# Optimization experiments

Hardware: AMD Instinct MI355X
Metric: run time of the kernel (lower is better)

The kernel has to match this reference:

```python
import jax, jax.numpy as jnp
import numpy as np

N_HEAD = 16

def setup_inputs() -> dict:
    key = jax.random.key(0)
    k1, k2, k3 = jax.random.split(key, 3)
    B, K, C = 2, 2048, 1024
    x = jax.random.normal(k1, (B, K, C), dtype=jnp.float32)
    W_qkv = jax.random.normal(k2, (C, 3 * C), dtype=jnp.float32) * (1.0 / np.sqrt(C))
    b_qkv = jnp.zeros((3 * C,), dtype=jnp.float32)
    W_proj = jax.random.normal(k3, (C, C), dtype=jnp.float32) * (1.0 / np.sqrt(C))
    b_proj = jnp.zeros((C,), dtype=jnp.float32)
    return {"x": x, "W_qkv": W_qkv, "b_qkv": b_qkv, "W_proj": W_proj, "b_proj": b_proj, "K": K}

def reference(x, W_qkv, b_qkv, W_proj, b_proj, K):
    B, _, C = x.shape
    H = N_HEAD
    Dh = C // H
    qkv = x @ W_qkv + b_qkv                      # [B, K, 3C]
    q, k, v = jnp.split(qkv, 3, axis=-1)
    # [B, H, K, Dh]
    q = q.reshape(B, K, H, Dh).transpose(0, 2, 1, 3)
    k = k.reshape(B, K, H, Dh).transpose(0, 2, 1, 3)
    v = v.reshape(B, K, H, Dh).transpose(0, 2, 1, 3)
    att = jnp.einsum('bhqd,bhkd->bhqk', q, k) / jnp.sqrt(jnp.asarray(Dh, dtype=x.dtype))
    causal = jnp.tril(jnp.ones((K, K), dtype=bool))
    att = jnp.where(causal[None, None], att, jnp.asarray(-jnp.inf, dtype=x.dtype))
    att = jax.nn.softmax(att, axis=-1)
    y = jnp.einsum('bhqk,bhkd->bhqd', att, v)    # [B, H, K, Dh]
    y = y.transpose(0, 2, 1, 3).reshape(B, K, C)
    return y @ W_proj + b_proj
```

## Files before the change

kernel.cpp:

```cpp
#include <hip/hip_runtime.h>
#include <hip/hip_bf16.h>
#include <math.h>

typedef __attribute__((ext_vector_type(8))) short short8;
typedef __attribute__((ext_vector_type(4))) float f32x4;
typedef __attribute__((ext_vector_type(4))) short short4v;
typedef __attribute__((ext_vector_type(2))) int int2v;

static __device__ __forceinline__ short f2bf(float f) {
    __hip_bfloat16 h = __float2bfloat16(f);
    return *reinterpret_cast<short*>(&h);
}
static __device__ __forceinline__ void store_out(float* p, float v) { *p = v; }
static __device__ __forceinline__ void store_out(short* p, float v) { *p = f2bf(v); }

#define GLL16(g, l) __builtin_amdgcn_global_load_lds( \
    (const __attribute__((address_space(1))) void*)(g), \
    (__attribute__((address_space(3))) void*)(l), 16, 0, 0)

#if __has_builtin(__builtin_amdgcn_exp2f)
#define EXP2(x) __builtin_amdgcn_exp2f(x)
#else
#define EXP2(x) exp2f(x)
#endif

#if __has_builtin(__builtin_amdgcn_cvt_pk_bf16_f32)
typedef __attribute__((ext_vector_type(2))) __bf16 bf16x2;
static __device__ __forceinline__ int pack2bf(float a, float b) {
    bf16x2 r = __builtin_amdgcn_cvt_pk_bf16_f32(a, b);
    return __builtin_bit_cast(int, r);
}
#else
static __device__ __forceinline__ int pack2bf(float a, float b) {
    unsigned ua = __builtin_bit_cast(unsigned, a) + 0x8000u;
    unsigned ub = __builtin_bit_cast(unsigned, b) + 0x8000u;
    return (int)((ua >> 16) | (ub & 0xFFFF0000u));
}
#endif

struct BTrue  { static constexpr bool v = true;  };
struct BFalse { static constexpr bool v = false; };

__global__ __launch_bounds__(256) void cast_bf16_kernel(
    const float* __restrict__ in, short* __restrict__ out, int n)
{
    int i = (blockIdx.x * 256 + threadIdx.x) * 4;
    if (i >= n) return;
    float4 v = *(const float4*)(in + i);
    short4v o = { f2bf(v.x), f2bf(v.y), f2bf(v.z), f2bf(v.w) };
    *(short4v*)(out + i) = o;
}

__global__ __launch_bounds__(256) void transpose_cast_kernel(
    const float* __restrict__ W, short* __restrict__ Wt, int Kd, int N)
{
    __shared__ float ts[32][33];
    const int c0 = blockIdx.x * 32, r0 = blockIdx.y * 32;
    const int tx = threadIdx.x & 31, ty = threadIdx.x >> 5;
    #pragma unroll
    for (int e = 0; e < 4; ++e)
        ts[ty + e * 8][tx] = W[(size_t)(r0 + ty + e * 8) * N + c0 + tx];
    __syncthreads();
    #pragma unroll
    for (int e = 0; e < 4; ++e)
        Wt[(size_t)(c0 + ty + e * 8) * Kd + r0 + tx] = f2bf(ts[tx][ty + e * 8]);
}

__global__ __launch_bounds__(256) void vtrans_kernel(
    const short* __restrict__ qkvb, short* __restrict__ vt, int K, int C)
{
    __shared__ short Vs[64][72];
    const int k0 = blockIdx.x * 64, h = blockIdx.y, b = blockIdx.z;
    const size_t rs = (size_t)3 * C;
    const short* src = qkvb + (size_t)b * K * rs + 2 * C + h * 64;
    const int key = threadIdx.x >> 3, d0 = (threadIdx.x & 7) * 8;
    *(short8*)&Vs[key][d0]      = *(const short8*)(src + (size_t)(k0 + key) * rs + d0);
    *(short8*)&Vs[key + 32][d0] = *(const short8*)(src + (size_t)(k0 + key + 32) * rs + d0);
    __syncthreads();
    const int d = threadIdx.x >> 2, kc = threadIdx.x & 3;
    short* dst = vt + ((size_t)(b * 16 + h) * 64 + d) * K + k0 + kc * 16;
    short8 o0, o1;
    #pragma unroll
    for (int j = 0; j < 8; ++j) { o0[j] = Vs[kc * 16 + j][d]; o1[j] = Vs[kc * 16 + 8 + j][d]; }
    *(short8*)dst = o0;
    *(short8*)(dst + 8) = o1;
}

#define GM 128
#define GN 128
#define GK 32

template <typename OutT>
__global__ __launch_bounds__(256) void gemm_mfma_kernel(
    const short* __restrict__ A, const short* __restrict__ Bt,
    const float* __restrict__ bias, OutT* __restrict__ C,
    int M, int N, int Kd)
{
    __shared__ __attribute__((aligned(16))) short As[GM * GK];
    __shared__ __attribute__((aligned(16))) short Bs[GN * GK];
    const int tid  = threadIdx.x;
    const int lane = tid & 63, w = tid >> 6;
    const int col  = lane & 15, quad = lane >> 4;
    const int wm = (w & 1) * 64, wn = (w >> 1) * 64;
    const int row0 = blockIdx.y * GM, col0 = blockIdx.x * GN;

    const int sr = tid >> 2, sc = (tid & 3) * 8;
    const short* gA = A  + (size_t)(row0 + sr) * Kd + sc;
    const short* gB = Bt + (size_t)(col0 + sr) * Kd + sc;
    short* lA = As + sr * GK + sc;
    short* lB = Bs + sr * GK + sc;
    const size_t skip = (size_t)64 * Kd;

    f32x4 acc[4][4] = {};
    for (int k0 = 0; k0 < Kd; k0 += GK) {
        __syncthreads();
        GLL16(gA,        lA);
        GLL16(gA + skip, lA + 64 * GK);
        GLL16(gB,        lB);
        GLL16(gB + skip, lB + 64 * GK);
        gA += GK; gB += GK;
        __syncthreads();

        short8 aF[4], bF[4];
        #pragma unroll
        for (int mt = 0; mt < 4; ++mt)
            aF[mt] = *(const short8*)&As[(wm + mt * 16 + col) * GK + quad * 8];
        #pragma unroll
        for (int nt = 0; nt < 4; ++nt)
            bF[nt] = *(const short8*)&Bs[(wn + nt * 16 + col) * GK + quad * 8];
        #pragma unroll
        for (int mt = 0; mt < 4; ++mt)
            #pragma unroll
            for (int nt = 0; nt < 4; ++nt)
                acc[mt][nt] = __builtin_amdgcn_mfma_f32_16x16x32_bf16(aF[mt], bF[nt], acc[mt][nt], 0, 0, 0);
    }

    #pragma unroll
    for (int mt = 0; mt < 4; ++mt)
        #pragma unroll
        for (int i = 0; i < 4; ++i) {
            const size_t r = row0 + wm + mt * 16 + quad * 4 + i;
            #pragma unroll
            for (int nt = 0; nt < 4; ++nt) {
                const int c = col0 + wn + nt * 16 + col;
                store_out(&C[r * N + c], acc[mt][nt][i] + bias[c]);
            }
        }
}

#define DH 64
#define FKT 64

__global__ __launch_bounds__(256) void flash_mfma_kernel(
    const short* __restrict__ qkvb,
    const short* __restrict__ vt,
    short* __restrict__ y,
    int K, int C)
{
    __shared__ __attribute__((aligned(16))) short Ks2[2 * 64 * 32];
    __shared__ __attribute__((aligned(16))) short Vs2[2 * 64 * 32];
    __shared__ __attribute__((aligned(16))) short Pt[4][16][72];

    const int tid  = threadIdx.x;
    const int lane = tid & 63, w = tid >> 6;
    const int col  = lane & 15, quad = lane >> 4;

    const int cmb  = blockIdx.x & 31;
    const int g    = blockIdx.x >> 5;
    const int b    = cmb >> 4, h = cmb & 15;
    const int NT   = K / 64;
    const float C2 = 0.18033688f;

    short8 bOnes;
    #pragma unroll
    for (int j = 0; j < 8; ++j) bOnes[j] = (col == 0) ? (short)0x3F80 : (short)0;

    const size_t rs = (size_t)3 * C;
    const short* qbase = qkvb + (size_t)b * K * rs + h * DH;
    const short* kbase = qbase + C;
    const short* vbase = vt + (size_t)(b * 16 + h) * DH * K;

    auto run = [&](int t0) {
        const int q0 = t0 + w * 16;

        short8 aQ0, aQ1;
        {
            const short* qp = qbase + (size_t)(q0 + col) * rs;
            aQ0 = *(const short8*)(qp + quad * 8);
            aQ1 = *(const short8*)(qp + 32 + quad * 8);
        }
        f32x4 O[4] = {};
        f32x4 L4 = {};

        const int nkt = t0 / FKT + 1;
        for (int it = 0; it < nkt; ++it) {
            const int kt = it * FKT;
            __syncthreads();
            #pragma unroll
            for (int cc = 0; cc < 2; ++cc) {
                const int seg  = w + 4 * cc;
                const int half = seg >> 2, kseg = seg & 3;
                const int rowl = kseg * 16 + (lane >> 2);
                const int grow = rowl ^ ((rowl >> 2) & 3);
                const int off  = half * 32 + (lane & 3) * 8;
                GLL16(kbase + (size_t)(kt + grow) * rs + off, &Ks2[seg * 512 + lane * 8]);
                GLL16(vbase + (size_t)rowl * K + kt + off,    &Vs2[seg * 512 + lane * 8]);
            }
            __syncthreads();

            f32x4 S[4] = {};
            #pragma unroll
            for (int nb = 0; nb < 4; ++nb) {
                const int prow = (col * 4 + nb) ^ (col & 3);
                short8 b0 = *(const short8*)&Ks2[prow * 32 + quad * 8];
                short8 b1 = *(const short8*)&Ks2[2048 + prow * 32 + quad * 8];
                S[nb] = __builtin_amdgcn_mfma_f32_16x16x32_bf16(aQ0, b0, S[nb], 0, 0, 0);
                S[nb] = __builtin_amdgcn_mfma_f32_16x16x32_bf16(aQ1, b1, S[nb], 0, 0, 0);
            }

            auto smax = [&](auto tag) {
                constexpr bool MASKED = decltype(tag)::v;
                #pragma unroll
                for (int i = 0; i < 4; ++i) {
                    const int q = q0 + quad * 4 + i;
                    float sv0 = S[0][i], sv1 = S[1][i], sv2 = S[2][i], sv3 = S[3][i];
                    if constexpr (MASKED) {
                        const int kc4 = kt + col * 4;
                        sv0 = (kc4 + 0 <= q) ? sv0 : -INFINITY;
                        sv1 = (kc4 + 1 <= q) ? sv1 : -INFINITY;
                        sv2 = (kc4 + 2 <= q) ? sv2 : -INFINITY;
                        sv3 = (kc4 + 3 <= q) ? sv3 : -INFINITY;
                    }
                    const float p0 = EXP2(sv0 * C2);
                    const float p1 = EXP2(sv1 * C2);
                    const float p2 = EXP2(sv2 * C2);
                    const float p3 = EXP2(sv3 * C2);
                    int2v pw = { pack2bf(p0, p1), pack2bf(p2, p3) };
                    *(int2v*)&Pt[w][quad * 4 + i][col * 4] = pw;
                }
            };
            if (kt + 63 <= q0) smax(BFalse{}); else smax(BTrue{});

            asm volatile("s_waitcnt lgkmcnt(0)" ::: "memory");

            #pragma unroll
            for (int half = 0; half < 2; ++half) {
                short8 aP = *(const short8*)&Pt[w][col][half * 32 + quad * 8];
                #pragma unroll
                for (int db = 0; db < 4; ++db) {
                    short8 bV = *(const short8*)&Vs2[half * 2048 + (db * 16 + col) * 32 + quad * 8];
                    O[db] = __builtin_amdgcn_mfma_f32_16x16x32_bf16(aP, bV, O[db], 0, 0, 0);
                }
                L4 = __builtin_amdgcn_mfma_f32_16x16x32_bf16(aP, bOnes, L4, 0, 0, 0);
            }
        }

        #pragma unroll
        for (int i = 0; i < 4; ++i) {
            const float l = __shfl(L4[i], quad * 16, 64);
            const float inv = 1.f / l;
            const int q = q0 + quad * 4 + i;
            short* yr = y + ((size_t)b * K + q) * C + h * DH;
            #pragma unroll
            for (int db = 0; db < 4; ++db)
                yr[db * 16 + col] = f2bf(O[db][i] * inv);
        }
    };

    run(g * 64);
    run((NT - 1 - g) * 64);
}

extern "C" void kernel_launch(void* const* d_in, const int* in_sizes, int n_in,
                              void* d_out, int out_size, void* d_ws, size_t ws_size,
                              hipStream_t stream)
{
    const float* x      = (const float*)d_in[0];
    const float* W_qkv  = (const float*)d_in[1];
    const float* b_qkv  = (const float*)d_in[2];
    const float* W_proj = (const float*)d_in[3];
    const float* b_proj = (const float*)d_in[4];

    const int B = 2, K = 2048, C = 1024, H = 16;
    const int M = B * K;

    char* ws = (char*)d_ws;
    short* xb    = (short*)ws;  ws += (size_t)M * C * 2;
    short* Wt1   = (short*)ws;  ws += (size_t)3 * C * C * 2;
    short* Wt2   = (short*)ws;  ws += (size_t)C * C * 2;
    short* qkvb  = (short*)ws;  ws += (size_t)M * 3 * C * 2;
    short* yb    = (short*)ws;  ws += (size_t)M * C * 2;
    short* vtb   = (short*)ws;

    cast_bf16_kernel<<<(M * C) / (256 * 4), 256, 0, stream>>>(x, xb, M * C);
    dim3 gt1((3 * C) / 32, C / 32);
    transpose_cast_kernel<<<gt1, 256, 0, stream>>>(W_qkv, Wt1, C, 3 * C);
    dim3 gt2(C / 32, C / 32);
    transpose_cast_kernel<<<gt2, 256, 0, stream>>>(W_proj, Wt2, C, C);

    dim3 g1((3 * C) / GN, M / GM);
    gemm_mfma_kernel<short><<<g1, 256, 0, stream>>>(xb, Wt1, b_qkv, qkvb, M, 3 * C, C);

    dim3 gv(K / 64, H, B);
    vtrans_kernel<<<gv, 256, 0, stream>>>(qkvb, vtb, K, C);

    const int NPAIR = (K / 64) / 2;
    flash_mfma_kernel<<<dim3(NPAIR * 32), 256, 0, stream>>>(qkvb, vtb, yb, K, C);

    dim3 g3(C / GN, M / GM);
    gemm_mfma_kernel<float><<<g3, 256, 0, stream>>>(yb, Wt2, b_proj, (float*)d_out, M, C, C);
}
```

Measured before the change: 194.5 us.

## Fuse prep kernels, fold softmax scale into QKV GEMM, widen flash warps to 32 queries

Merges the three input cast/transpose kernels into one launch to cut launch overhead. Folds the softmax scale (log2e/sqrt(Dh)) into the Q columns of the QKV GEMM epilogue, so the per-element multiply in the flash loop goes away. Restructures the flash kernel to 128 threads with each warp handling 32 query rows, so K/V fragments loaded from LDS are reused across two query groups. The cost is more registers per thread and fewer waves per block, which could hurt latency hiding; Q is also rounded to bf16 after scaling.

Result: slower. 207.3 us (+6.6%).

```diff
diff --git a/kernel.cpp b/kernel.cpp
--- a/kernel.cpp
+++ b/kernel.cpp
@@ -41,21 +41,12 @@
 struct BTrue  { static constexpr bool v = true;  };
 struct BFalse { static constexpr bool v = false; };
 
-__global__ __launch_bounds__(256) void cast_bf16_kernel(
-    const float* __restrict__ in, short* __restrict__ out, int n)
-{
-    int i = (blockIdx.x * 256 + threadIdx.x) * 4;
-    if (i >= n) return;
-    float4 v = *(const float4*)(in + i);
-    short4v o = { f2bf(v.x), f2bf(v.y), f2bf(v.z), f2bf(v.w) };
-    *(short4v*)(out + i) = o;
-}
-
-__global__ __launch_bounds__(256) void transpose_cast_kernel(
-    const float* __restrict__ W, short* __restrict__ Wt, int Kd, int N)
+static __device__ __forceinline__ void transpose_cast_tile(
+    const float* __restrict__ W, short* __restrict__ Wt, int Kd, int N,
+    int bx, int by)
 {
     __shared__ float ts[32][33];
-    const int c0 = blockIdx.x * 32, r0 = blockIdx.y * 32;
+    const int c0 = bx * 32, r0 = by * 32;
     const int tx = threadIdx.x & 31, ty = threadIdx.x >> 5;
     #pragma unroll
     for (int e = 0; e < 4; ++e)
@@ -64,6 +55,35 @@
     #pragma unroll
     for (int e = 0; e < 4; ++e)
         Wt[(size_t)(c0 + ty + e * 8) * Kd + r0 + tx] = f2bf(ts[tx][ty + e * 8]);
+}
+
+__global__ __launch_bounds__(256) void prep_kernel(
+    const float* __restrict__ x,      short* __restrict__ xb,    int nx,
+    const float* __restrict__ W_qkv,  short* __restrict__ Wt1,
+    const float* __restrict__ W_proj, short* __restrict__ Wt2,
+    int C)
+{
+    const int nbx = nx / 1024;
+    const int nb1 = (3 * C / 32) * (C / 32);
+    int bid = blockIdx.x;
+    if (bid < nbx) {
+        int i = (bid * 256 + threadIdx.x) * 4;
+        float4 v = *(const float4*)(x + i);
+        short4v o = { f2bf(v.x), f2bf(v.y), f2bf(v.z), f2bf(v.w) };
+        *(short4v*)(xb + i) = o;
+        return;
+    }
+    bid -= nbx;
+    if (bid < nb1) {
+        const int nc = 3 * C / 32;
+        transpose_cast_tile(W_qkv, Wt1, C, 3 * C, bid % nc, bid / nc);
+        return;
+    }
+    bid -= nb1;
+    {
+        const int nc = C / 32;
+        transpose_cast_tile(W_proj, Wt2, C, C, bid % nc, bid / nc);
+    }
 }
 
 __global__ __launch_bounds__(256) void vtrans_kernel(
@@ -94,7 +114,7 @@
 __global__ __launch_bounds__(256) void gemm_mfma_kernel(
     const short* __restrict__ A, const short* __restrict__ Bt,
     const float* __restrict__ bias, OutT* __restrict__ C,
-    int M, int N, int Kd)
+    int M, int N, int Kd, int qcols, float qscale)
 {
     __shared__ __attribute__((aligned(16))) short As[GM * GK];
     __shared__ __attribute__((aligned(16))) short Bs[GN * GK];
@@ -103,12 +123,13 @@
     const int col  = lane & 15, quad = lane >> 4;
     const int wm = (w & 1) * 64, wn = (w >> 1) * 64;
     const int row0 = blockIdx.y * GM, col0 = blockIdx.x * GN;
-
-    const int sr = tid >> 2, sc = (tid & 3) * 8;
-    const short* gA = A  + (size_t)(row0 + sr) * Kd + sc;
-    const short* gB = Bt + (size_t)(col0 + sr) * Kd + sc;
-    short* lA = As + sr * GK + sc;
-    short* lB = Bs + sr * GK + sc;
+    const float sc = (col0 < qcols) ? qscale : 1.f;
+
+    const int sr = tid >> 2, scg = (tid & 3) * 8;
+    const short* gA = A  + (size_t)(row0 + sr) * Kd + scg;
+    const short* gB = Bt + (size_t)(col0 + sr) * Kd + scg;
+    short* lA = As + sr * GK + scg;
+    short* lB = Bs + sr * GK + scg;
     const size_t skip = (size_t)64 * Kd;
 
     f32x4 acc[4][4] = {};
@@ -143,7 +164,7 @@
             #pragma unroll
             for (int nt = 0; nt < 4; ++nt) {
                 const int c = col0 + wn + nt * 16 + col;
-                store_out(&C[r * N + c], acc[mt][nt][i] + bias[c]);
+                store_out(&C[r * N + c], (acc[mt][nt][i] + bias[c]) * sc);
             }
         }
 }
@@ -151,7 +172,7 @@
 #define DH 64
 #define FKT 64
 
-__global__ __launch_bounds__(256) void flash_mfma_kernel(
+__global__ __launch_bounds__(128) void flash_mfma_kernel(
     const short* __restrict__ qkvb,
     const short* __restrict__ vt,
     short* __restrict__ y,
@@ -159,7 +180,7 @@
 {
     __shared__ __attribute__((aligned(16))) short Ks2[2 * 64 * 32];
     __shared__ __attribute__((aligned(16))) short Vs2[2 * 64 * 32];
-    __shared__ __attribute__((aligned(16))) short Pt[4][16][72];
+    __shared__ __attribute__((aligned(16))) short Pt[2][32][72];
 
     const int tid  = threadIdx.x;
     const int lane = tid & 63, w = tid >> 6;
@@ -169,7 +190,6 @@
     const int g    = blockIdx.x >> 5;
     const int b    = cmb >> 4, h = cmb & 15;
     const int NT   = K / 64;
-    const float C2 = 0.18033688f;
 
     short8 bOnes;
     #pragma unroll
@@ -181,24 +201,25 @@
     const short* vbase = vt + (size_t)(b * 16 + h) * DH * K;
 
     auto run = [&](int t0) {
-        const int q0 = t0 + w * 16;
-
-        short8 aQ0, aQ1;
-        {
-            const short* qp = qbase + (size_t)(q0 + col) * rs;
-            aQ0 = *(const short8*)(qp + quad * 8);
-            aQ1 = *(const short8*)(qp + 32 + quad * 8);
+        const int q0 = t0 + w * 32;
+
+        short8 aQ[2][2];
+        #pragma unroll
+        for (int qg = 0; qg < 2; ++qg) {
+            const short* qp = qbase + (size_t)(q0 + qg * 16 + col) * rs;
+            aQ[qg][0] = *(const short8*)(qp + quad * 8);
+            aQ[qg][1] = *(const short8*)(qp + 32 + quad * 8);
         }
-        f32x4 O[4] = {};
-        f32x4 L4 = {};
+        f32x4 O[2][4] = {};
+        f32x4 L4[2] = {};
 
         const int nkt = t0 / FKT + 1;
         for (int it = 0; it < nkt; ++it) {
             const int kt = it * FKT;
             __syncthreads();
             #pragma unroll
-            for (int cc = 0; cc < 2; ++cc) {
-                const int seg  = w + 4 * cc;
+            for (int cc = 0; cc < 4; ++cc) {
+                const int seg  = w * 4 + cc;
                 const int half = seg >> 2, kseg = seg & 3;
                 const int rowl = kseg * 16 + (lane >> 2);
                 const int grow = rowl ^ ((rowl >> 2) & 3);
@@ -208,63 +229,78 @@
             }
             __syncthreads();
 
-            f32x4 S[4] = {};
+            short8 bK[4][2], bV[4][2];
             #pragma unroll
             for (int nb = 0; nb < 4; ++nb) {
                 const int prow = (col * 4 + nb) ^ (col & 3);
-                short8 b0 = *(const short8*)&Ks2[prow * 32 + quad * 8];
-                short8 b1 = *(const short8*)&Ks2[2048 + prow * 32 + quad * 8];
-                S[nb] = __builtin_amdgcn_mfma_f32_16x16x32_bf16(aQ0, b0, S[nb], 0, 0, 0);
-                S[nb] = __builtin_amdgcn_mfma_f32_16x16x32_bf16(aQ1, b1, S[nb], 0, 0, 0);
-            }
-
-            auto smax = [&](auto tag) {
-                constexpr bool MASKED = decltype(tag)::v;
+                bK[nb][0] = *(const short8*)&Ks2[prow * 32 + quad * 8];
+                bK[nb][1] = *(const short8*)&Ks2[2048 + prow * 32 + quad * 8];
+            }
+            #pragma unroll
+            for (int db = 0; db < 4; ++db) {
+                bV[db][0] = *(const short8*)&Vs2[(db * 16 + col) * 32 + quad * 8];
+                bV[db][1] = *(const short8*)&Vs2[2048 + (db * 16 + col) * 32 + quad * 8];
+            }
+
+            #pragma unroll
+            for (int qg = 0; qg < 2; ++qg) {
+                const int qb = q0 + qg * 16;
+
+                f32x4 S[4] = {};
                 #pragma unroll
-                for (int i = 0; i < 4; ++i) {
-                    const int q = q0 + quad * 4 + i;
-                    float sv0 = S[0][i], sv1 = S[1][i], sv2 = S[2][i], sv3 = S[3][i];
-                    if constexpr (MASKED) {
-                        const int kc4 = kt + col * 4;
-                        sv0 = (kc4 + 0 <= q) ? sv0 : -INFINITY;
-                        sv1 = (kc4 + 1 <= q) ? sv1 : -INFINITY;
-                        sv2 = (kc4 + 2 <= q) ? sv2 : -INFINITY;
-                        sv3 = (kc4 + 3 <= q) ? sv3 : -INFINITY;
+                for (int nb = 0; nb < 4; ++nb) {
+                    S[nb] = __builtin_amdgcn_mfma_f32_16x16x32_bf16(aQ[qg][0], bK[nb][0], S[nb], 0, 0, 0);
+                    S[nb] = __builtin_amdgcn_mfma_f32_16x16x32_bf16(aQ[qg][1], bK[nb][1], S[nb], 0, 0, 0);
+                }
+
+                auto smax = [&](auto tag) {
+                    constexpr bool MASKED = decltype(tag)::v;
+                    #pragma unroll
+                    for (int i = 0; i < 4; ++i) {
+                        const int q = qb + quad * 4 + i;
+                        float sv0 = S[0][i], sv1 = S[1][i], sv2 = S[2][i], sv3 = S[3][i];
+                        if constexpr (MASKED) {
+                            const int kc4 = kt + col * 4;
+                            sv0 = (kc4 + 0 <= q) ? sv0 : -INFINITY;
+                            sv1 = (kc4 + 1 <= q) ? sv1 : -INFINITY;
+                            sv2 = (kc4 + 2 <= q) ? sv2 : -INFINITY;
+                            sv3 = (kc4 + 3 <= q) ? sv3 : -INFINITY;
+                        }
+                        const float p0 = EXP2(sv0);
+                        const float p1 = EXP2(sv1);
+                        const float p2 = EXP2(sv2);
+                        const float p3 = EXP2(sv3);
+                        int2v pw = { pack2bf(p0, p1), pack2bf(p2, p3) };
+                        *(int2v*)&Pt[w][qg * 16 + quad * 4 + i][col * 4] = pw;
                     }
-                    const float p0 = EXP2(sv0 * C2);
-                    const float p1 = EXP2(sv1 * C2);
-                    const float p2 = EXP2(sv2 * C2);
-                    const float p3 = EXP2(sv3 * C2);
-                    int2v pw = { pack2bf(p0, p1), pack2bf(p2, p3) };
-                    *(int2v*)&Pt[w][quad * 4 + i][col * 4] = pw;
+                };
+                if (kt + 63 <= qb) smax(BFalse{}); else smax(BTrue{});
+
+                asm volatile("s_waitcnt lgkmcnt(0)" ::: "memory");
+
+                #pragma unroll
+                for (int half = 0; half < 2; ++half) {
+                    short8 aP = *(const short8*)&Pt[w][qg * 16 + col][half * 32 + quad * 8];
+                    #pragma unroll
+                    for (int db = 0; db < 4; ++db)
+                        O[qg][db] = __builtin_amdgcn_mfma_f32_16x16x32_bf16(aP, bV[db][half], O[qg][db], 0, 0, 0);
+                    L4[qg] = __builtin_amdgcn_mfma_f32_16x16x32_bf16(aP, bOnes, L4[qg], 0, 0, 0);
                 }
-            };
-            if (kt + 63 <= q0) smax(BFalse{}); else smax(BTrue{});
-
-            asm volatile("s_waitcnt lgkmcnt(0)" ::: "memory");
-
-            #pragma unroll
-            for (int half = 0; half < 2; ++half) {
-                short8 aP = *(const short8*)&Pt[w][col][half * 32 + quad * 8];
+            }
+        }
+
+        #pragma unroll
+        for (int qg = 0; qg < 2; ++qg)
+            #pragma unroll
+            for (int i = 0; i < 4; ++i) {
+                const float l = __shfl(L4[qg][i], quad * 16, 64);
+                const float inv = 1.f / l;
+                const int q = q0 + qg * 16 + quad * 4 + i;
+                short* yr = y + ((size_t)b * K + q) * C + h * DH;
                 #pragma unroll
-                for (int db = 0; db < 4; ++db) {
-                    short8 bV = *(const short8*)&Vs2[half * 2048 + (db * 16 + col) * 32 + quad * 8];
-                    O[db] = __builtin_amdgcn_mfma_f32_16x16x32_bf16(aP, bV, O[db], 0, 0, 0);
-                }
-                L4 = __builtin_amdgcn_mfma_f32_16x16x32_bf16(aP, bOnes, L4, 0, 0, 0);
-            }
-        }
-
-        #pragma unroll
-        for (int i = 0; i < 4; ++i) {
-            const float l = __shfl(L4[i], quad * 16, 64);
-            const float inv = 1.f / l;
-            const int q = q0 + quad * 4 + i;
-            short* yr = y + ((size_t)b * K + q) * C + h * DH;
-            #pragma unroll
-            for (int db = 0; db < 4; ++db)
-                yr[db * 16 + col] = f2bf(O[db][i] * inv);
-        }
+                for (int db = 0; db < 4; ++db)
+                    yr[db * 16 + col] = f2bf(O[qg][db][i] * inv);
+            }
     };
 
     run(g * 64);
@@ -283,6 +319,7 @@
 
     const int B = 2, K = 2048, C = 1024, H = 16;
     const int M = B * K;
+    const float C2 = 0.18033688f;
 
     char* ws = (char*)d_ws;
     short* xb    = (short*)ws;  ws += (size_t)M * C * 2;
@@ -292,21 +329,20 @@
     short* yb    = (short*)ws;  ws += (size_t)M * C * 2;
     short* vtb   = (short*)ws;
 
-    cast_bf16_kernel<<<(M * C) / (256 * 4), 256, 0, stream>>>(x, xb, M * C);
-    dim3 gt1((3 * C) / 32, C / 32);
-    transpose_cast_kernel<<<gt1, 256, 0, stream>>>(W_qkv, Wt1, C, 3 * C);
-    dim3 gt2(C / 32, C / 32);
-    transpose_cast_kernel<<<gt2, 256, 0, stream>>>(W_proj, Wt2, C, C);
+    const int nbx = (M * C) / 1024;
+    const int nb1 = (3 * C / 32) * (C / 32);
+    const int nb2 = (C / 32) * (C / 32);
+    prep_kernel<<<nbx + nb1 + nb2, 256, 0, stream>>>(x, xb, M * C, W_qkv, Wt1, W_proj, Wt2, C);
 
     dim3 g1((3 * C) / GN, M / GM);
-    gemm_mfma_kernel<short><<<g1, 256, 0, stream>>>(xb, Wt1, b_qkv, qkvb, M, 3 * C, C);
+    gemm_mfma_kernel<short><<<g1, 256, 0, stream>>>(xb, Wt1, b_qkv, qkvb, M, 3 * C, C, C, C2);
 
     dim3 gv(K / 64, H, B);
     vtrans_kernel<<<gv, 256, 0, stream>>>(qkvb, vtb, K, C);
 
     const int NPAIR = (K / 64) / 2;
-    flash_mfma_kernel<<<dim3(NPAIR * 32), 256, 0, stream>>>(qkvb, vtb, yb, K, C);
+    flash_mfma_kernel<<<dim3(NPAIR * 32), 128, 0, stream>>>(qkvb, vtb, yb, K, C);
 
     dim3 g3(C / GN, M / GM);
-    gemm_mfma_kernel<float><<<g3, 256, 0, stream>>>(yb, Wt2, b_proj, (float*)d_out, M, C, C);
-}
+    gemm_mfma_kernel<float><<<g3, 256, 0, stream>>>(yb, Wt2, b_proj, (float*)d_out, M, C, C, 0, 1.f);
+}
```
